# Optimization experiments

Hardware: AMD Instinct MI355X
Metric: run time of the kernel (lower is better)

## Reference

```python
import jax, jax.numpy as jnp
import numpy as np

B, S, HID = 1, 2048, 4096
NH, NKV, HD = 32, 8, 128
GROUPS = NH // NKV
ROPE_THETA = 10000.0


def rotate_half(x):
    x1, x2 = jnp.split(x, 2, axis=-1)
    return jnp.concatenate([-x2, x1], axis=-1)


def rope_cos_sin(position_ids, head_dim, dtype):
    # inv_freq: [hd/2]; position_ids: [B, S]
    inv_freq = 1.0 / (ROPE_THETA ** (jnp.arange(0, head_dim, 2, dtype=jnp.float32) / head_dim))
    freqs = position_ids.astype(jnp.float32)[..., None] * inv_freq  # [B, S, hd/2]
    emb = jnp.concatenate([freqs, freqs], axis=-1)                  # [B, S, hd]
    return jnp.cos(emb).astype(dtype), jnp.sin(emb).astype(dtype)


def apply_rope(x, cos, sin):
    # x: [B, H, S, hd]; cos/sin: [B, S, hd] -> broadcast over heads
    return x * cos[:, None] + rotate_half(x) * sin[:, None]


def setup_inputs() -> dict:
    key = jax.random.key(0)
    ks = jax.random.split(key, 5)
    scale = 0.02
    return {
        "hidden_states": jax.random.normal(ks[0], (B, S, HID), dtype=jnp.float32),
        "wq": jax.random.normal(ks[1], (HID, NH * HD), dtype=jnp.float32) * scale,
        "wk": jax.random.normal(ks[2], (HID, NKV * HD), dtype=jnp.float32) * scale,
        "wv": jax.random.normal(ks[3], (HID, NKV * HD), dtype=jnp.float32) * scale,
        "wo": jax.random.normal(ks[4], (NH * HD, HID), dtype=jnp.float32) * scale,
        "position_ids": jnp.arange(S, dtype=jnp.int32)[None, :],
    }


def reference(hidden_states, wq, wk, wv, wo, position_ids):
    bsz, q_len, _ = hidden_states.shape
    # projections (nn.Linear, bias=False)
    q = (hidden_states @ wq).reshape(bsz, q_len, NH, HD).transpose(0, 2, 1, 3)   # [B,NH,S,hd]
    k = (hidden_states @ wk).reshape(bsz, q_len, NKV, HD).transpose(0, 2, 1, 3)  # [B,NKV,S,hd]
    v = (hidden_states @ wv).reshape(bsz, q_len, NKV, HD).transpose(0, 2, 1, 3)
    # RoPE applied to Q and K at global positions (prefill: no past cache)
    cos, sin = rope_cos_sin(position_ids, HD, q.dtype)
    q = apply_rope(q, cos, sin)
    k = apply_rope(k, cos, sin)
    # GQA: expand KV heads to query heads
    k_full = jnp.repeat(k, GROUPS, axis=1)  # [B,NH,S,hd]
    v_full = jnp.repeat(v, GROUPS, axis=1)
    # prefill flash attention == causal SDPA
    logits = jnp.einsum('bhqd,bhkd->bhqk', q, k_full) / jnp.sqrt(jnp.asarray(HD, q.dtype))
    causal = jnp.tril(jnp.ones((q_len, q_len), dtype=bool))
    neg = jnp.asarray(jnp.finfo(q.dtype).min, q.dtype)
    logits = jnp.where(causal[None, None], logits, neg)
    probs = jax.nn.softmax(logits, axis=-1)                     # [B,NH,S,S]
    attn = jnp.einsum('bhqk,bhkd->bhqd', probs, v_full)          # [B,NH,S,hd]
    attn_output = attn.transpose(0, 2, 1, 3).reshape(bsz, q_len, NH * HD) @ wo
    # chunked prefill eviction scores: causal attention probs accumulated over
    # all queries, aggregated per KV head group -> [B, NKV, kv_len]
    accumulated_scores = probs.sum(axis=2).reshape(bsz, NKV, GROUPS, q_len).sum(axis=2)
    return attn_output, accumulated_scores
```

## Files before the change

kernel.cpp:

```cpp
#include <hip/hip_runtime.h>
#include <hip/hip_bf16.h>
#include <cstdint>
#include <cstddef>

#define S_LEN 2048
#define HID_DIM 4096
#define NH 32
#define NKV 8
#define HD 128
#define LOG2E 1.4426950408889634f
#define SCALE 0.08838834764831845f

typedef __attribute__((ext_vector_type(8))) short bf16x8;
typedef __attribute__((ext_vector_type(4))) float f32x4;
typedef __attribute__((ext_vector_type(4))) short short4v;

__device__ __forceinline__ short f2bf(float f) {
  union { float f; unsigned u; } v; v.f = f;
  return (short)((v.u + 0x7fffu + ((v.u >> 16) & 1u)) >> 16);
}
__device__ __forceinline__ float bf2f(short s) {
  union { unsigned u; float f; } v; v.u = ((unsigned)(unsigned short)s) << 16;
  return v.f;
}
__device__ __forceinline__ void gld_lds16(const void* g, void* l) {
  __builtin_amdgcn_global_load_lds((const __attribute__((address_space(1))) unsigned*)g,
                                   (__attribute__((address_space(3))) unsigned*)l, 16, 0, 0);
}

__global__ void cvt_kernel(const float* __restrict__ in, short* __restrict__ out, int n) {
  int i = (blockIdx.x * 256 + threadIdx.x) * 4;
  if (i < n) {
    float4 f = *(const float4*)(in + i);
    short4v o = { f2bf(f.x), f2bf(f.y), f2bf(f.z), f2bf(f.w) };
    *(short4v*)(out + i) = o;
  }
}

__global__ void tconv_kernel(const float* __restrict__ in, short* __restrict__ out, int R, int C) {
  __shared__ float tile[32][33];
  int tr = blockIdx.y * 32, tc = blockIdx.x * 32;
  int tx = threadIdx.x & 31, ty = threadIdx.x >> 5;
#pragma unroll
  for (int i = 0; i < 32; i += 8)
    tile[ty + i][tx] = in[(size_t)(tr + ty + i) * C + tc + tx];
  __syncthreads();
#pragma unroll
  for (int i = 0; i < 32; i += 8)
    out[(size_t)(tc + ty + i) * R + tr + tx] = f2bf(tile[tx][ty + i]);
}

template<int MODE>
__global__ __launch_bounds__(256, 2) void gemm_bt_kernel(
    const short* __restrict__ A, const short* __restrict__ Bt,
    void* __restrict__ Cout, int M, int N, int K, int nbx)
{
  __shared__ short As[128 * 32];
  __shared__ short Bs[128 * 32];
  const int tid = threadIdx.x;
  const int lane = tid & 63;
  const int w = tid >> 6;
  const int wm = w >> 1, wn = w & 1;
  const int q8 = gridDim.x >> 3;
  const int lin = (blockIdx.x & 7) * q8 + (blockIdx.x >> 3);
  const int by = lin / nbx, bx = lin - by * nbx;
  const int m0 = by * 128, n0 = bx * 128;

  f32x4 acc[4][4];
#pragma unroll
  for (int i = 0; i < 4; i++)
#pragma unroll
    for (int j = 0; j < 4; j++) acc[i][j] = (f32x4){0.f, 0.f, 0.f, 0.f};

  for (int k0 = 0; k0 < K; k0 += 32) {
    __syncthreads();
#pragma unroll
    for (int rep = 0; rep < 2; rep++) {
      int c = rep * 256 + w * 64 + lane;
      int row = c >> 2, slot = c & 3;
      int gs = slot ^ (row & 3);
      gld_lds16(A + (size_t)(m0 + row) * K + k0 + gs * 8, As + c * 8);
      gld_lds16(Bt + (size_t)(n0 + row) * K + k0 + gs * 8, Bs + c * 8);
    }
    __syncthreads();
    bf16x8 af[4], bf[4];
#pragma unroll
    for (int ms = 0; ms < 4; ms++) {
      int row = wm * 64 + ms * 16 + (lane & 15);
      af[ms] = *(const bf16x8*)(As + row * 32 + (((lane >> 4) ^ (row & 3)) << 3));
    }
#pragma unroll
    for (int ns = 0; ns < 4; ns++) {
      int row = wn * 64 + ns * 16 + (lane & 15);
      bf[ns] = *(const bf16x8*)(Bs + row * 32 + (((lane >> 4) ^ (row & 3)) << 3));
    }
#pragma unroll
    for (int ms = 0; ms < 4; ms++)
#pragma unroll
      for (int ns = 0; ns < 4; ns++)
        acc[ms][ns] = __builtin_amdgcn_mfma_f32_16x16x32_bf16(af[ms], bf[ns], acc[ms][ns], 0, 0, 0);
  }

#pragma unroll
  for (int ms = 0; ms < 4; ms++) {
    int mb = m0 + wm * 64 + ms * 16 + ((lane >> 4) << 2);
#pragma unroll
    for (int ns = 0; ns < 4; ns++) {
      int n = n0 + wn * 64 + ns * 16 + (lane & 15);
      if (MODE == 3) {
        short* o = (short*)Cout;
        if (n < NH * HD) {
          int head = n >> 7, d = n & 127;
#pragma unroll
          for (int r = 0; r < 4; r++)
            o[((size_t)head * M + (mb + r)) * HD + d] = f2bf(acc[ms][ns][r]);
        } else if (n < (NH + NKV) * HD) {
          int head = (n - NH * HD) >> 7, d = n & 127;
          short* ok = o + (size_t)NH * S_LEN * HD;
#pragma unroll
          for (int r = 0; r < 4; r++)
            ok[((size_t)head * M + (mb + r)) * HD + d] = f2bf(acc[ms][ns][r]);
        } else {
          int head = (n - (NH + NKV) * HD) >> 7, d = n & 127;
          short* ov = o + (size_t)(NH + NKV) * S_LEN * HD;
          short4v pk;
#pragma unroll
          for (int r = 0; r < 4; r++) pk[r] = f2bf(acc[ms][ns][r]);
          *(short4v*)(ov + ((size_t)head * HD + d) * M + mb) = pk;
        }
      } else {
        float* o = (float*)Cout;
#pragma unroll
        for (int r = 0; r < 4; r++)
          o[(size_t)(mb + r) * N + n] = acc[ms][ns][r];
      }
    }
  }
}

__global__ void rope_kernel(short* __restrict__ q, short* __restrict__ k,
                            const int* __restrict__ pos_ids) {
  const int s = blockIdx.x;
  const int hh = blockIdx.y * 4 + threadIdx.y;
  const int d = threadIdx.x;
  const float pos = (float)pos_ids[s];
  const float inv = __expf(-(float)d * 0.14391157f);
  float sn, c;
  __sincosf(pos * inv, &sn, &c);
  short* base = (hh < NH) ? (q + ((size_t)hh * S_LEN + s) * HD)
                          : (k + ((size_t)(hh - NH) * S_LEN + s) * HD);
  float x1 = bf2f(base[d]), x2 = bf2f(base[d + 64]);
  base[d] = f2bf(x1 * c - x2 * sn);
  base[d + 64] = f2bf(x2 * c + x1 * sn);
}

__global__ __launch_bounds__(512, 4) void attn_kernel(
    const short* __restrict__ Qr, const short* __restrict__ Kr, const short* __restrict__ Vt,
    short* __restrict__ attn_out, float* __restrict__ scores)
{
  __shared__ short Ks[64 * 128];
  __shared__ short Vs[128 * 64];

  const int tid = threadIdx.x;
  const int lane = tid & 63;
  const int w = tid >> 6;
  const int hi = lane >> 4;
  const int ql = lane & 15;
  const int lin = (blockIdx.x & 7) * 64 + (blockIdx.x >> 3);
  const int h = lin >> 4;
  const int qt = 15 - (lin & 15);
  const int kvh = h >> 2;
  const int qbase = qt * 128 + w * 16;
  const int qglob = qbase + ql;
  const int qmax = qbase + 15;
  const int ntiles = 2 * qt + 2;
  const float CS = SCALE * LOG2E;

  bf16x8 qf[4];
  {
    const short* qrow = Qr + ((size_t)h * S_LEN + qglob) * HD + hi * 8;
#pragma unroll
    for (int kc = 0; kc < 4; kc++) qf[kc] = *(const bf16x8*)(qrow + kc * 32);
  }

  f32x4 oacc[8];
#pragma unroll
  for (int i = 0; i < 8; i++) oacc[i] = (f32x4){0.f, 0.f, 0.f, 0.f};
  float lsum = 0.f;

  for (int t = 0; t < ntiles; t++) {
    const int kb = t * 64;
    __syncthreads();
#pragma unroll
    for (int rep = 0; rep < 2; rep++) {
      int c = rep * 512 + tid;
      int x = c >> 4, slot = c & 15;
      int key = (x & 32) | ((x & 16) >> 2) | ((x & 12) << 1) | (x & 3);
      int gs = slot ^ (x & 7);
      gld_lds16(Kr + ((size_t)kvh * S_LEN + kb + key) * HD + gs * 8, Ks + c * 8);
    }
#pragma unroll
    for (int rep = 0; rep < 2; rep++) {
      int c = rep * 512 + tid;
      int d = c >> 3, slot = c & 7;
      int gs = slot ^ (d & 7);
      gld_lds16(Vt + ((size_t)kvh * HD + d) * S_LEN + kb + gs * 8, Vs + c * 8);
    }
    __syncthreads();
    if (kb > qmax) continue;

    f32x4 sf[4];
#pragma unroll
    for (int g = 0; g < 4; g++) sf[g] = (f32x4){0.f, 0.f, 0.f, 0.f};
    __builtin_amdgcn_s_setprio(1);
#pragma unroll
    for (int g = 0; g < 4; g++)
#pragma unroll
      for (int kc = 0; kc < 4; kc++) {
        int row = g * 16 + ql;
        bf16x8 kf = *(const bf16x8*)(Ks + row * 128 + (((kc * 4 + hi) ^ (ql & 7)) << 3));
        sf[g] = __builtin_amdgcn_mfma_f32_16x16x32_bf16(kf, qf[kc], sf[g], 0, 0, 0);
      }
    __builtin_amdgcn_s_setprio(0);

    const bool diag = (kb + 63 > qbase);
    bf16x8 pa[2];
#pragma unroll
    for (int kh = 0; kh < 2; kh++)
#pragma unroll
      for (int j = 0; j < 2; j++) {
        int g = 2 * kh + j;
        int kbase = kb + kh * 32 + j * 4 + hi * 8;
#pragma unroll
        for (int r = 0; r < 4; r++) {
          float p = exp2f(sf[g][r] * CS);
          if (diag && (kbase + r > qglob)) p = 0.f;
          lsum += p;
          pa[kh][j * 4 + r] = f2bf(p);
        }
      }

    __builtin_amdgcn_s_setprio(1);
#pragma unroll
    for (int ds = 0; ds < 8; ds++) {
      int d = ds * 16 + ql;
#pragma unroll
      for (int kh = 0; kh < 2; kh++) {
        bf16x8 vf = *(const bf16x8*)(Vs + d * 64 + (((kh * 4 + hi) ^ (d & 7)) << 3));
        oacc[ds] = __builtin_amdgcn_mfma_f32_16x16x32_bf16(pa[kh], vf, oacc[ds], 0, 0, 0);
      }
    }
    __builtin_amdgcn_s_setprio(0);
  }

  lsum += __shfl_xor(lsum, 16);
  lsum += __shfl_xor(lsum, 32);
  float rl[4];
#pragma unroll
  for (int r = 0; r < 4; r++) rl[r] = 1.f / __shfl(lsum, hi * 4 + r);

#pragma unroll
  for (int ds = 0; ds < 8; ds++)
#pragma unroll
    for (int r = 0; r < 4; r++) {
      int qq = qbase + hi * 4 + r;
      int d = ds * 16 + ql;
      attn_out[(size_t)qq * HID_DIM + h * HD + d] = f2bf(oacc[ds][r] * rl[r]);
    }

  float* cs = (float*)Vs;
  __syncthreads();
  for (int i = tid; i < 2048; i += 512) cs[i] = 0.f;

  for (int t = 0; t < ntiles; t++) {
    const int kb = t * 64;
    __syncthreads();
#pragma unroll
    for (int rep = 0; rep < 2; rep++) {
      int c = rep * 512 + tid;
      int x = c >> 4, slot = c & 15;
      int key = (x & 32) | ((x & 16) >> 2) | ((x & 12) << 1) | (x & 3);
      int gs = slot ^ (x & 7);
      gld_lds16(Kr + ((size_t)kvh * S_LEN + kb + key) * HD + gs * 8, Ks + c * 8);
    }
    __syncthreads();
    if (kb > qmax) continue;

    f32x4 sg[4];
#pragma unroll
    for (int c = 0; c < 4; c++) sg[c] = (f32x4){0.f, 0.f, 0.f, 0.f};
    __builtin_amdgcn_s_setprio(1);
#pragma unroll
    for (int c = 0; c < 4; c++)
#pragma unroll
      for (int kc = 0; kc < 4; kc++) {
        int row = c * 16 + ql;
        bf16x8 kf = *(const bf16x8*)(Ks + row * 128 + (((kc * 4 + hi) ^ (ql & 7)) << 3));
        sg[c] = __builtin_amdgcn_mfma_f32_16x16x32_bf16(qf[kc], kf, sg[c], 0, 0, 0);
      }
    __builtin_amdgcn_s_setprio(0);

    const bool diag = (kb + 63 > qbase);
#pragma unroll
    for (int c = 0; c < 4; c++) {
      int key = kb + ((c >> 1) << 5) + ((c & 1) << 2) + ((ql >> 2) << 3) + (ql & 3);
      float sum = 0.f;
#pragma unroll
      for (int r = 0; r < 4; r++) {
        float p = exp2f(sg[c][r] * CS) * rl[r];
        if (diag && (key > qbase + hi * 4 + r)) p = 0.f;
        sum += p;
      }
      sum += __shfl_xor(sum, 16);
      sum += __shfl_xor(sum, 32);
      if (lane < 16) atomicAdd(&cs[key], sum);
    }
  }

  __syncthreads();
  const int nk = ntiles * 64;
  for (int i = tid; i < nk; i += 512)
    atomicAdd(scores + (size_t)kvh * S_LEN + i, cs[i]);
}

extern "C" void kernel_launch(void* const* d_in, const int* in_sizes, int n_in,
                              void* d_out, int out_size, void* d_ws, size_t ws_size,
                              hipStream_t stream) {
  const float* hs = (const float*)d_in[0];
  const float* wq = (const float*)d_in[1];
  const float* wk = (const float*)d_in[2];
  const float* wv = (const float*)d_in[3];
  const float* wo = (const float*)d_in[4];
  const int* pos = (const int*)d_in[5];
  float* out = (float*)d_out;

  char* ws = (char*)d_ws;
  const size_t off_hs   = 0;
  const size_t off_wqT  = off_hs   + (size_t)S_LEN * HID_DIM * 2;
  const size_t off_wkT  = off_wqT  + (size_t)HID_DIM * HID_DIM * 2;
  const size_t off_wvT  = off_wkT  + (size_t)1024 * HID_DIM * 2;
  const size_t off_woT  = off_wvT  + (size_t)1024 * HID_DIM * 2;
  const size_t off_Qr   = off_woT  + (size_t)HID_DIM * HID_DIM * 2;
  const size_t off_Kr   = off_Qr   + (size_t)NH * S_LEN * HD * 2;
  const size_t off_Vt   = off_Kr   + (size_t)NKV * S_LEN * HD * 2;
  const size_t off_attn = off_Vt   + (size_t)NKV * HD * S_LEN * 2;

  short* hsb  = (short*)(ws + off_hs);
  short* wqT  = (short*)(ws + off_wqT);
  short* wkT  = (short*)(ws + off_wkT);
  short* wvT  = (short*)(ws + off_wvT);
  short* woT  = (short*)(ws + off_woT);
  short* Qr   = (short*)(ws + off_Qr);
  short* Kr   = (short*)(ws + off_Kr);
  short* Vt   = (short*)(ws + off_Vt);
  short* attb = (short*)(ws + off_attn);

  cvt_kernel<<<dim3((S_LEN * HID_DIM) / 1024), 256, 0, stream>>>(hs, hsb, S_LEN * HID_DIM);
  tconv_kernel<<<dim3(128, 128), 256, 0, stream>>>(wq, wqT, HID_DIM, HID_DIM);
  tconv_kernel<<<dim3(32, 128), 256, 0, stream>>>(wk, wkT, HID_DIM, 1024);
  tconv_kernel<<<dim3(32, 128), 256, 0, stream>>>(wv, wvT, HID_DIM, 1024);
  tconv_kernel<<<dim3(128, 128), 256, 0, stream>>>(wo, woT, HID_DIM, HID_DIM);

  gemm_bt_kernel<3><<<768, 256, 0, stream>>>(hsb, wqT, Qr, S_LEN, 6144, HID_DIM, 48);

  rope_kernel<<<dim3(S_LEN, 10), dim3(64, 4), 0, stream>>>(Qr, Kr, pos);

  hipMemsetAsync(out + (size_t)S_LEN * HID_DIM, 0, (size_t)NKV * S_LEN * sizeof(float), stream);
  attn_kernel<<<512, 512, 0, stream>>>(Qr, Kr, Vt, attb, out + (size_t)S_LEN * HID_DIM);

  gemm_bt_kernel<2><<<512, 256, 0, stream>>>(attb, woT, out, S_LEN, HID_DIM, HID_DIM, 32);
}
```

Measured before the change: 456.5 us.

## Double-buffer K/V loads and pair causal query tiles per attention block

Result: faster. 398.7 us (-12.7%).

```diff
diff --git a/kernel.cpp b/kernel.cpp
--- a/kernel.cpp
+++ b/kernel.cpp
@@ -14,6 +14,7 @@
 typedef __attribute__((ext_vector_type(8))) short bf16x8;
 typedef __attribute__((ext_vector_type(4))) float f32x4;
 typedef __attribute__((ext_vector_type(4))) short short4v;
+typedef __attribute__((ext_vector_type(4))) unsigned u32x4;
 
 __device__ __forceinline__ short f2bf(float f) {
   union { float f; unsigned u; } v; v.f = f;
@@ -23,10 +24,19 @@
   union { unsigned u; float f; } v; v.u = ((unsigned)(unsigned short)s) << 16;
   return v.f;
 }
+__device__ __forceinline__ unsigned cvt_pk_bf16(float lo, float hi) {
+  unsigned r;
+  asm("v_cvt_pk_bf16_f32 %0, %1, %2" : "=v"(r) : "v"(lo), "v"(hi));
+  return r;
+}
 __device__ __forceinline__ void gld_lds16(const void* g, void* l) {
   __builtin_amdgcn_global_load_lds((const __attribute__((address_space(1))) unsigned*)g,
                                    (__attribute__((address_space(3))) unsigned*)l, 16, 0, 0);
 }
+
+#define WAITVM4() asm volatile("s_waitcnt vmcnt(4)" ::: "memory")
+#define WAITVM2() asm volatile("s_waitcnt vmcnt(2)" ::: "memory")
+#define WAITVM0() asm volatile("s_waitcnt vmcnt(0)" ::: "memory")
 
 __global__ void cvt_kernel(const float* __restrict__ in, short* __restrict__ out, int n) {
   int i = (blockIdx.x * 256 + threadIdx.x) * 4;
@@ -154,171 +164,215 @@
   base[d + 64] = f2bf(x2 * c + x1 * sn);
 }
 
-__global__ __launch_bounds__(512, 4) void attn_kernel(
+__global__ __launch_bounds__(512, 2) void attn_kernel(
     const short* __restrict__ Qr, const short* __restrict__ Kr, const short* __restrict__ Vt,
     short* __restrict__ attn_out, float* __restrict__ scores)
 {
-  __shared__ short Ks[64 * 128];
-  __shared__ short Vs[128 * 64];
+  __shared__ short Ks[2][64 * 128];
+  __shared__ short Vs[2][128 * 64];
+  __shared__ float cs[2048];
 
   const int tid = threadIdx.x;
   const int lane = tid & 63;
   const int w = tid >> 6;
   const int hi = lane >> 4;
   const int ql = lane & 15;
-  const int lin = (blockIdx.x & 7) * 64 + (blockIdx.x >> 3);
-  const int h = lin >> 4;
-  const int qt = 15 - (lin & 15);
+  const int lin = (blockIdx.x & 7) * 32 + (blockIdx.x >> 3);
+  const int h = lin >> 3;
+  const int pr = lin & 7;
   const int kvh = h >> 2;
-  const int qbase = qt * 128 + w * 16;
-  const int qglob = qbase + ql;
-  const int qmax = qbase + 15;
-  const int ntiles = 2 * qt + 2;
   const float CS = SCALE * LOG2E;
 
-  bf16x8 qf[4];
-  {
-    const short* qrow = Qr + ((size_t)h * S_LEN + qglob) * HD + hi * 8;
-#pragma unroll
-    for (int kc = 0; kc < 4; kc++) qf[kc] = *(const bf16x8*)(qrow + kc * 32);
-  }
-
-  f32x4 oacc[8];
-#pragma unroll
-  for (int i = 0; i < 8; i++) oacc[i] = (f32x4){0.f, 0.f, 0.f, 0.f};
-  float lsum = 0.f;
-
-  for (int t = 0; t < ntiles; t++) {
-    const int kb = t * 64;
-    __syncthreads();
+  const short* KrB = Kr + (size_t)kvh * S_LEN * HD;
+  const short* VtB = Vt + (size_t)kvh * HD * S_LEN;
+
+  for (int i = tid; i < 2048; i += 512) cs[i] = 0.f;
+
+  auto stageKV = [&](int bb, int t) {
+    const int kb2 = t * 64;
 #pragma unroll
     for (int rep = 0; rep < 2; rep++) {
       int c = rep * 512 + tid;
       int x = c >> 4, slot = c & 15;
       int key = (x & 32) | ((x & 16) >> 2) | ((x & 12) << 1) | (x & 3);
       int gs = slot ^ (x & 7);
-      gld_lds16(Kr + ((size_t)kvh * S_LEN + kb + key) * HD + gs * 8, Ks + c * 8);
+      gld_lds16(KrB + (size_t)(kb2 + key) * HD + gs * 8, &Ks[bb][c * 8]);
     }
 #pragma unroll
     for (int rep = 0; rep < 2; rep++) {
       int c = rep * 512 + tid;
       int d = c >> 3, slot = c & 7;
       int gs = slot ^ (d & 7);
-      gld_lds16(Vt + ((size_t)kvh * HD + d) * S_LEN + kb + gs * 8, Vs + c * 8);
-    }
-    __syncthreads();
-    if (kb > qmax) continue;
-
-    f32x4 sf[4];
-#pragma unroll
-    for (int g = 0; g < 4; g++) sf[g] = (f32x4){0.f, 0.f, 0.f, 0.f};
-    __builtin_amdgcn_s_setprio(1);
-#pragma unroll
-    for (int g = 0; g < 4; g++)
-#pragma unroll
-      for (int kc = 0; kc < 4; kc++) {
-        int row = g * 16 + ql;
-        bf16x8 kf = *(const bf16x8*)(Ks + row * 128 + (((kc * 4 + hi) ^ (ql & 7)) << 3));
-        sf[g] = __builtin_amdgcn_mfma_f32_16x16x32_bf16(kf, qf[kc], sf[g], 0, 0, 0);
-      }
-    __builtin_amdgcn_s_setprio(0);
-
-    const bool diag = (kb + 63 > qbase);
-    bf16x8 pa[2];
-#pragma unroll
-    for (int kh = 0; kh < 2; kh++)
-#pragma unroll
-      for (int j = 0; j < 2; j++) {
-        int g = 2 * kh + j;
-        int kbase = kb + kh * 32 + j * 4 + hi * 8;
-#pragma unroll
-        for (int r = 0; r < 4; r++) {
-          float p = exp2f(sf[g][r] * CS);
-          if (diag && (kbase + r > qglob)) p = 0.f;
-          lsum += p;
-          pa[kh][j * 4 + r] = f2bf(p);
-        }
-      }
-
-    __builtin_amdgcn_s_setprio(1);
-#pragma unroll
-    for (int ds = 0; ds < 8; ds++) {
-      int d = ds * 16 + ql;
-#pragma unroll
-      for (int kh = 0; kh < 2; kh++) {
-        bf16x8 vf = *(const bf16x8*)(Vs + d * 64 + (((kh * 4 + hi) ^ (d & 7)) << 3));
-        oacc[ds] = __builtin_amdgcn_mfma_f32_16x16x32_bf16(pa[kh], vf, oacc[ds], 0, 0, 0);
-      }
-    }
-    __builtin_amdgcn_s_setprio(0);
-  }
-
-  lsum += __shfl_xor(lsum, 16);
-  lsum += __shfl_xor(lsum, 32);
-  float rl[4];
-#pragma unroll
-  for (int r = 0; r < 4; r++) rl[r] = 1.f / __shfl(lsum, hi * 4 + r);
-
-#pragma unroll
-  for (int ds = 0; ds < 8; ds++)
-#pragma unroll
-    for (int r = 0; r < 4; r++) {
-      int qq = qbase + hi * 4 + r;
-      int d = ds * 16 + ql;
-      attn_out[(size_t)qq * HID_DIM + h * HD + d] = f2bf(oacc[ds][r] * rl[r]);
-    }
-
-  float* cs = (float*)Vs;
-  __syncthreads();
-  for (int i = tid; i < 2048; i += 512) cs[i] = 0.f;
-
-  for (int t = 0; t < ntiles; t++) {
-    const int kb = t * 64;
-    __syncthreads();
+      gld_lds16(VtB + (size_t)d * S_LEN + kb2 + gs * 8, &Vs[bb][c * 8]);
+    }
+  };
+  auto stageK = [&](int bb, int t) {
+    const int kb2 = t * 64;
 #pragma unroll
     for (int rep = 0; rep < 2; rep++) {
       int c = rep * 512 + tid;
       int x = c >> 4, slot = c & 15;
       int key = (x & 32) | ((x & 16) >> 2) | ((x & 12) << 1) | (x & 3);
       int gs = slot ^ (x & 7);
-      gld_lds16(Kr + ((size_t)kvh * S_LEN + kb + key) * HD + gs * 8, Ks + c * 8);
-    }
-    __syncthreads();
-    if (kb > qmax) continue;
-
-    f32x4 sg[4];
-#pragma unroll
-    for (int c = 0; c < 4; c++) sg[c] = (f32x4){0.f, 0.f, 0.f, 0.f};
-    __builtin_amdgcn_s_setprio(1);
-#pragma unroll
-    for (int c = 0; c < 4; c++)
-#pragma unroll
-      for (int kc = 0; kc < 4; kc++) {
-        int row = c * 16 + ql;
-        bf16x8 kf = *(const bf16x8*)(Ks + row * 128 + (((kc * 4 + hi) ^ (ql & 7)) << 3));
-        sg[c] = __builtin_amdgcn_mfma_f32_16x16x32_bf16(qf[kc], kf, sg[c], 0, 0, 0);
+      gld_lds16(KrB + (size_t)(kb2 + key) * HD + gs * 8, &Ks[bb][c * 8]);
+    }
+  };
+
+  int maxnt = 0;
+
+  for (int sidx = 0; sidx < 2; sidx++) {
+    const int qt = sidx ? (15 - pr) : pr;
+    const int nt = 2 * qt + 2;
+    if (nt > maxnt) maxnt = nt;
+    const int qbase = qt * 128 + w * 16;
+    const int qglob = qbase + ql;
+    const int qmax = qbase + 15;
+
+    bf16x8 qf[4];
+    {
+      const short* qrow = Qr + ((size_t)h * S_LEN + qglob) * HD + hi * 8;
+#pragma unroll
+      for (int kc = 0; kc < 4; kc++) qf[kc] = *(const bf16x8*)(qrow + kc * 32);
+    }
+
+    f32x4 oacc[8];
+#pragma unroll
+    for (int i = 0; i < 8; i++) oacc[i] = (f32x4){0.f, 0.f, 0.f, 0.f};
+    float lsum = 0.f;
+
+    stageKV(0, 0);
+    for (int t = 0; t < nt; t++) {
+      const int b = t & 1;
+      const int kb = t * 64;
+      if (t + 1 < nt) { stageKV(b ^ 1, t + 1); WAITVM4(); }
+      else            { WAITVM0(); }
+      __builtin_amdgcn_s_barrier();
+
+      if (kb <= qmax) {
+        f32x4 sf[4];
+#pragma unroll
+        for (int g = 0; g < 4; g++) sf[g] = (f32x4){0.f, 0.f, 0.f, 0.f};
+        __builtin_amdgcn_s_setprio(1);
+#pragma unroll
+        for (int g = 0; g < 4; g++)
+#pragma unroll
+          for (int kc = 0; kc < 4; kc++) {
+            int row = g * 16 + ql;
+            bf16x8 kf = *(const bf16x8*)(&Ks[b][row * 128 + (((kc * 4 + hi) ^ (ql & 7)) << 3)]);
+            sf[g] = __builtin_amdgcn_mfma_f32_16x16x32_bf16(kf, qf[kc], sf[g], 0, 0, 0);
+          }
+        __builtin_amdgcn_s_setprio(0);
+
+        float p[4][4];
+#pragma unroll
+        for (int g = 0; g < 4; g++)
+#pragma unroll
+          for (int r = 0; r < 4; r++) p[g][r] = exp2f(sf[g][r] * CS);
+        if (kb + 63 > qbase) {
+#pragma unroll
+          for (int g = 0; g < 4; g++)
+#pragma unroll
+            for (int r = 0; r < 4; r++) {
+              int key = kb + ((g >> 1) << 5) + ((g & 1) << 2) + (hi << 3) + r;
+              if (key > qglob) p[g][r] = 0.f;
+            }
+        }
+#pragma unroll
+        for (int g = 0; g < 4; g++)
+#pragma unroll
+          for (int r = 0; r < 4; r++) lsum += p[g][r];
+
+        bf16x8 pa[2];
+#pragma unroll
+        for (int kh = 0; kh < 2; kh++) {
+          u32x4 pw;
+          pw[0] = cvt_pk_bf16(p[2 * kh][0], p[2 * kh][1]);
+          pw[1] = cvt_pk_bf16(p[2 * kh][2], p[2 * kh][3]);
+          pw[2] = cvt_pk_bf16(p[2 * kh + 1][0], p[2 * kh + 1][1]);
+          pw[3] = cvt_pk_bf16(p[2 * kh + 1][2], p[2 * kh + 1][3]);
+          pa[kh] = __builtin_bit_cast(bf16x8, pw);
+        }
+
+        __builtin_amdgcn_s_setprio(1);
+#pragma unroll
+        for (int ds = 0; ds < 8; ds++) {
+          int d = ds * 16 + ql;
+#pragma unroll
+          for (int kh = 0; kh < 2; kh++) {
+            bf16x8 vf = *(const bf16x8*)(&Vs[b][d * 64 + (((kh * 4 + hi) ^ (d & 7)) << 3)]);
+            oacc[ds] = __builtin_amdgcn_mfma_f32_16x16x32_bf16(pa[kh], vf, oacc[ds], 0, 0, 0);
+          }
+        }
+        __builtin_amdgcn_s_setprio(0);
       }
-    __builtin_amdgcn_s_setprio(0);
-
-    const bool diag = (kb + 63 > qbase);
-#pragma unroll
-    for (int c = 0; c < 4; c++) {
-      int key = kb + ((c >> 1) << 5) + ((c & 1) << 2) + ((ql >> 2) << 3) + (ql & 3);
-      float sum = 0.f;
+      __builtin_amdgcn_s_barrier();
+    }
+
+    lsum += __shfl_xor(lsum, 16);
+    lsum += __shfl_xor(lsum, 32);
+    float rl[4];
+#pragma unroll
+    for (int r = 0; r < 4; r++) rl[r] = 1.f / __shfl(lsum, hi * 4 + r);
+
+#pragma unroll
+    for (int ds = 0; ds < 8; ds++)
 #pragma unroll
       for (int r = 0; r < 4; r++) {
-        float p = exp2f(sg[c][r] * CS) * rl[r];
-        if (diag && (key > qbase + hi * 4 + r)) p = 0.f;
-        sum += p;
+        int qq = qbase + hi * 4 + r;
+        int d = ds * 16 + ql;
+        attn_out[(size_t)qq * HID_DIM + h * HD + d] = f2bf(oacc[ds][r] * rl[r]);
       }
-      sum += __shfl_xor(sum, 16);
-      sum += __shfl_xor(sum, 32);
-      if (lane < 16) atomicAdd(&cs[key], sum);
+
+    stageK(0, 0);
+    for (int t = 0; t < nt; t++) {
+      const int b = t & 1;
+      const int kb = t * 64;
+      if (t + 1 < nt) { stageK(b ^ 1, t + 1); WAITVM2(); }
+      else            { WAITVM0(); }
+      __builtin_amdgcn_s_barrier();
+
+      if (kb <= qmax) {
+        f32x4 sg[4];
+#pragma unroll
+        for (int c = 0; c < 4; c++) sg[c] = (f32x4){0.f, 0.f, 0.f, 0.f};
+        __builtin_amdgcn_s_setprio(1);
+#pragma unroll
+        for (int c = 0; c < 4; c++)
+#pragma unroll
+          for (int kc = 0; kc < 4; kc++) {
+            int row = c * 16 + ql;
+            bf16x8 kf = *(const bf16x8*)(&Ks[b][row * 128 + (((kc * 4 + hi) ^ (ql & 7)) << 3)]);
+            sg[c] = __builtin_amdgcn_mfma_f32_16x16x32_bf16(qf[kc], kf, sg[c], 0, 0, 0);
+          }
+        __builtin_amdgcn_s_setprio(0);
+
+        const bool diag = (kb + 63 > qbase);
+#pragma unroll
+        for (int c = 0; c < 4; c++) {
+          int key = kb + ((c >> 1) << 5) + ((c & 1) << 2) + ((ql >> 2) << 3) + (ql & 3);
+          float sum = 0.f;
+          if (diag) {
+#pragma unroll
+            for (int r = 0; r < 4; r++) {
+              float pv = exp2f(sg[c][r] * CS) * rl[r];
+              if (key > qbase + hi * 4 + r) pv = 0.f;
+              sum += pv;
+            }
+          } else {
+#pragma unroll
+            for (int r = 0; r < 4; r++) sum += exp2f(sg[c][r] * CS) * rl[r];
+          }
+          sum += __shfl_xor(sum, 16);
+          sum += __shfl_xor(sum, 32);
+          if (lane < 16) atomicAdd(&cs[key], sum);
+        }
+      }
+      __builtin_amdgcn_s_barrier();
     }
   }
 
-  __syncthreads();
-  const int nk = ntiles * 64;
+  __builtin_amdgcn_s_barrier();
+  const int nk = maxnt * 64;
   for (int i = tid; i < nk; i += 512)
     atomicAdd(scores + (size_t)kvh * S_LEN + i, cs[i]);
 }
@@ -366,7 +420,7 @@
   rope_kernel<<<dim3(S_LEN, 10), dim3(64, 4), 0, stream>>>(Qr, Kr, pos);
 
   hipMemsetAsync(out + (size_t)S_LEN * HID_DIM, 0, (size_t)NKV * S_LEN * sizeof(float), stream);
-  attn_kernel<<<512, 512, 0, stream>>>(Qr, Kr, Vt, attb, out + (size_t)S_LEN * HID_DIM);
+  attn_kernel<<<256, 512, 0, stream>>>(Qr, Kr, Vt, attb, out + (size_t)S_LEN * HID_DIM);
 
   gemm_bt_kernel<2><<<512, 256, 0, stream>>>(attb, woT, out, S_LEN, HID_DIM, HID_DIM, 32);
 }
```
